# Optimization experiments

Measured on AMD Instinct MI355X. Metric: run time of the kernel, lower is better.

The kernel has to match this reference:

```python
import jax, jax.numpy as jnp
import numpy as np

CHANNELS = [4096, 4096, 4096, 4096]
SPARSITY = 0.9  # fraction of weight entries zeroed (sten.random_mask_sparsify frac)
BATCH = 4096


def _sparse_weight(key, out_f, in_f, frac):
    kw, km = jax.random.split(key)
    w = jax.random.normal(kw, (out_f, in_f), dtype=jnp.float32)
    keep = jax.random.uniform(km, (out_f, in_f)) >= frac  # keep ~(1-frac) entries
    return jnp.where(keep, w, 0.0)


def setup_inputs() -> dict:
    key = jax.random.key(0)
    ks = jax.random.split(key, 7)
    x = jax.random.normal(ks[0], (BATCH, CHANNELS[0]), dtype=jnp.float32)
    W1 = _sparse_weight(ks[1], CHANNELS[1], CHANNELS[0], SPARSITY)
    b1 = jax.random.uniform(ks[2], (CHANNELS[1],), dtype=jnp.float32)
    W2 = _sparse_weight(ks[3], CHANNELS[2], CHANNELS[1], SPARSITY)
    b2 = jax.random.uniform(ks[4], (CHANNELS[2],), dtype=jnp.float32)
    W3 = _sparse_weight(ks[5], CHANNELS[3], CHANNELS[2], SPARSITY)
    b3 = jax.random.uniform(ks[6], (CHANNELS[3],), dtype=jnp.float32)
    return {"x": x, "W1": W1, "b1": b1, "W2": W2, "b2": b2, "W3": W3, "b3": b3}


def reference(x, W1, b1, W2, b2, W3, b3):
    # Sequential: Linear -> ReLU -> Linear -> ReLU -> Linear
    # F.linear(x, W, b) == x @ W.T + b; weights already carry the sparsity mask.
    h = x @ W1.T + b1
    h = jax.nn.relu(h)
    h = h @ W2.T + b2
    h = jax.nn.relu(h)
    return h @ W3.T + b3
```

## Files before the change

### kernel.cpp

```cpp
#include <hip/hip_runtime.h>
#include <cstdint>


#define MATN 4096
#define NT (MATN / 64)

typedef _Float16 half8 __attribute__((ext_vector_type(8)));
typedef float f32x4 __attribute__((ext_vector_type(4)));

__device__ __forceinline__ void glds16(const void* g, void* l) {
    __builtin_amdgcn_global_load_lds(
        (const __attribute__((address_space(1))) char*)(uintptr_t)g,
        (__attribute__((address_space(3))) char*)(uintptr_t)l,
        16, 0, 0);
}

__device__ __forceinline__ void cvt_body(const float* __restrict__ in,
                                         _Float16* __restrict__ out, int n8) {
    for (int g = blockIdx.x * 256 + threadIdx.x; g < n8; g += gridDim.x * 256) {
        size_t i = (size_t)g * 8;
        float4 a = *(const float4*)(in + i);
        float4 b = *(const float4*)(in + i + 4);
        half8 o;
        o[0] = (_Float16)a.x; o[1] = (_Float16)a.y;
        o[2] = (_Float16)a.z; o[3] = (_Float16)a.w;
        o[4] = (_Float16)b.x; o[5] = (_Float16)b.y;
        o[6] = (_Float16)b.z; o[7] = (_Float16)b.w;
        *(half8*)(out + i) = o;
    }
}

__global__ __launch_bounds__(256)
void cvt_f16(const float* __restrict__ in, _Float16* __restrict__ out, int n8) {
    cvt_body(in, out, n8);
}

__global__ __launch_bounds__(256)
void cvt_f16_2(const float* __restrict__ i0, _Float16* __restrict__ o0,
               const float* __restrict__ i1, _Float16* __restrict__ o1, int n8) {
    cvt_body(blockIdx.y ? i1 : i0, blockIdx.y ? o1 : o0, n8);
}

__global__ __launch_bounds__(256)
void cvt_f16_4(const float* __restrict__ i0, _Float16* __restrict__ o0,
               const float* __restrict__ i1, _Float16* __restrict__ o1,
               const float* __restrict__ i2, _Float16* __restrict__ o2,
               const float* __restrict__ i3, _Float16* __restrict__ o3, int n8) {
    const float* in;
    _Float16* out;
    switch (blockIdx.y) {
        case 0: in = i0; out = o0; break;
        case 1: in = i1; out = o1; break;
        case 2: in = i2; out = o2; break;
        default: in = i3; out = o3; break;
    }
    cvt_body(in, out, n8);
}

#define MFMA_(d, x, y) d = __builtin_amdgcn_mfma_f32_16x16x32_f16(x, y, d, 0, 0, 0)

template <bool RELU, typename OutT>
__global__ __launch_bounds__(512, 2)
void gemm_bt(const _Float16* __restrict__ A, const _Float16* __restrict__ B,
             const float* __restrict__ bias, OutT* __restrict__ C) {
    __shared__ _Float16 lds[2][4][128 * 64];

    const int tid  = threadIdx.x;
    const int lane = tid & 63;
    const int w    = tid >> 6;
    const int wm   = w >> 2;
    const int wn   = w & 3;
    const int l16  = lane & 15;
    const int kq   = lane >> 4;

    const int bid   = blockIdx.y * 16 + blockIdx.x;
    const int sbid  = (bid & 7) * 32 + (bid >> 3);
    const int tileM = (sbid >> 4) * 256;
    const int tileN = (sbid & 15) * 256;

    const int rin = tid >> 3;
    const int gch = (tid & 7) ^ (rin & 7);
    char* const ldsb = (char*)lds;
    const int wq = w * 1024;

    const _Float16* const arow = A + (size_t)(tileM + rin) * MATN + gch * 8;
    const _Float16* const brow = B + (size_t)(tileN + rin) * MATN + gch * 8;

#define STAGE(Tt, s, rowp, roff)                                               \
    do {                                                                       \
        if ((Tt) < NT) {                                                       \
            const _Float16* g_ = (rowp) + (size_t)(roff) * MATN + (Tt) * 64;   \
            char* l_ = ldsb + ((((Tt) & 1) * 4 + (s)) * 16384) + wq;           \
            glds16(g_, l_);                                                    \
            glds16(g_ + (size_t)64 * MATN, l_ + 8192);                         \
        }                                                                      \
    } while (0)

    const int rbA = (wm * 16 + l16) * 128;
    const int rbB = (wn * 16 + l16) * 128;
    const int ok0 = (kq ^ (l16 & 7)) * 16;
    const int ok1 = ok0 ^ 64;

    half8 aP[4], aQ[4], bP[4], bQ[4];
    f32x4 acc[8][4] = {};

    STAGE(0, 0, arow, 0);
    STAGE(0, 1, brow, 0);
    STAGE(0, 2, brow, 128);
    STAGE(0, 3, arow, 128);
    STAGE(1, 2, brow, 128);
    asm volatile("s_waitcnt vmcnt(2)" ::: "memory");
    __builtin_amdgcn_s_barrier();

#pragma unroll 2
    for (int T = 0; T < NT; ++T) {
        const char* base  = ldsb + (T & 1) * 65536;
        const char* bufA0 = base;
        const char* bufB0 = base + 16384;
        const char* bufB1 = base + 32768;
        const char* bufA1 = base + 49152;

#pragma unroll
        for (int mi = 0; mi < 4; ++mi)
            aP[mi] = *(const half8*)(bufA0 + mi * 4096 + rbA + ok0);
        bP[0] = *(const half8*)(bufB0 + rbB + ok0);
        bP[1] = *(const half8*)(bufB0 + 8192 + rbB + ok0);
        bP[2] = *(const half8*)(bufB1 + rbB + ok0);
        bP[3] = *(const half8*)(bufB1 + 8192 + rbB + ok0);
#pragma unroll
        for (int mi = 0; mi < 4; ++mi)
            aQ[mi] = *(const half8*)(bufA1 + mi * 4096 + rbA + ok0);
        STAGE(T + 1, 0, arow, 0);
        __builtin_amdgcn_s_barrier();
        asm volatile("s_waitcnt lgkmcnt(4)" ::: "memory");
        __builtin_amdgcn_sched_barrier(0);
        __builtin_amdgcn_s_setprio(1);
#pragma unroll
        for (int mi = 0; mi < 4; ++mi)
#pragma unroll
            for (int ni = 0; ni < 4; ++ni)
                MFMA_(acc[mi][ni], aP[mi], bP[ni]);
        __builtin_amdgcn_s_setprio(0);
        __builtin_amdgcn_s_barrier();

#pragma unroll
        for (int mi = 0; mi < 4; ++mi)
            aP[mi] = *(const half8*)(bufA1 + mi * 4096 + rbA + ok1);
        bQ[0] = *(const half8*)(bufB0 + rbB + ok1);
        bQ[1] = *(const half8*)(bufB0 + 8192 + rbB + ok1);
        bQ[2] = *(const half8*)(bufB1 + rbB + ok1);
        bQ[3] = *(const half8*)(bufB1 + 8192 + rbB + ok1);
        STAGE(T + 1, 3, arow, 128);
        __builtin_amdgcn_s_barrier();
        asm volatile("s_waitcnt lgkmcnt(8)" ::: "memory");
        __builtin_amdgcn_sched_barrier(0);
        __builtin_amdgcn_s_setprio(1);
#pragma unroll
        for (int mi = 0; mi < 4; ++mi)
#pragma unroll
            for (int ni = 0; ni < 4; ++ni)
                MFMA_(acc[4 + mi][ni], aQ[mi], bP[ni]);
        __builtin_amdgcn_s_setprio(0);
        __builtin_amdgcn_s_barrier();

#pragma unroll
        for (int mi = 0; mi < 4; ++mi)
            aQ[mi] = *(const half8*)(bufA0 + mi * 4096 + rbA + ok1);
        STAGE(T + 1, 1, brow, 0);
        __builtin_amdgcn_s_barrier();
        asm volatile("s_waitcnt lgkmcnt(4)" ::: "memory");
        __builtin_amdgcn_sched_barrier(0);
        __builtin_amdgcn_s_setprio(1);
#pragma unroll
        for (int mi = 0; mi < 4; ++mi)
#pragma unroll
            for (int ni = 0; ni < 4; ++ni)
                MFMA_(acc[4 + mi][ni], aP[mi], bQ[ni]);
        __builtin_amdgcn_s_setprio(0);
        __builtin_amdgcn_s_barrier();

        STAGE(T + 2, 2, brow, 128);
        __builtin_amdgcn_s_barrier();
        asm volatile("s_waitcnt lgkmcnt(0)" ::: "memory");
        __builtin_amdgcn_sched_barrier(0);
        __builtin_amdgcn_s_setprio(1);
#pragma unroll
        for (int mi = 0; mi < 4; ++mi)
#pragma unroll
            for (int ni = 0; ni < 4; ++ni)
                MFMA_(acc[mi][ni], aQ[mi], bQ[ni]);
        __builtin_amdgcn_s_setprio(0);
        if (T < NT - 2)
            asm volatile("s_waitcnt vmcnt(2)" ::: "memory");
        else
            asm volatile("s_waitcnt vmcnt(0)" ::: "memory");
        __builtin_amdgcn_s_barrier();
    }
#undef STAGE

#pragma unroll
    for (int ni = 0; ni < 4; ++ni) {
        const int gn = tileN + ni * 64 + wn * 16 + l16;
        const float bv = bias[gn];
#pragma unroll
        for (int mi = 0; mi < 8; ++mi) {
            const int gm = tileM + mi * 32 + wm * 16 + kq * 4;
#pragma unroll
            for (int r = 0; r < 4; ++r) {
                float v = acc[mi][ni][r] + bv;
                if (RELU) v = v > 0.f ? v : 0.f;
                C[(size_t)(gm + r) * MATN + gn] = (OutT)v;
            }
        }
    }
}

extern "C" void kernel_launch(void* const* d_in, const int* in_sizes, int n_in,
                              void* d_out, int out_size, void* d_ws, size_t ws_size,
                              hipStream_t stream) {
    const float* x  = (const float*)d_in[0];
    const float* W1 = (const float*)d_in[1];
    const float* b1 = (const float*)d_in[2];
    const float* W2 = (const float*)d_in[3];
    const float* b2 = (const float*)d_in[4];
    const float* W3 = (const float*)d_in[5];
    const float* b3 = (const float*)d_in[6];
    float* out = (float*)d_out;

    const size_t MAT = (size_t)MATN * MATN;
    const size_t HB  = MAT * 2;
    const int n8 = (int)(MAT / 8);
    dim3 ggrid(MATN / 256, MATN / 256);

    if (ws_size >= HB * 5) {
        _Float16* xb = (_Float16*)d_ws;
        _Float16* w1 = (_Float16*)((char*)d_ws + HB);
        _Float16* w2 = (_Float16*)((char*)d_ws + HB * 2);
        _Float16* w3 = (_Float16*)((char*)d_ws + HB * 3);
        _Float16* h1 = (_Float16*)((char*)d_ws + HB * 4);
        _Float16* h2 = xb;

        cvt_f16_4<<<dim3(2048, 4), 256, 0, stream>>>(x, xb, W1, w1, W2, w2,
                                                     W3, w3, n8);
        gemm_bt<true, _Float16><<<ggrid, 512, 0, stream>>>(xb, w1, b1, h1);
        gemm_bt<true, _Float16><<<ggrid, 512, 0, stream>>>(h1, w2, b2, h2);
        gemm_bt<false, float><<<ggrid, 512, 0, stream>>>(h2, w3, b3, out);
    } else {
        _Float16* xb = (_Float16*)d_ws;
        _Float16* wb = (_Float16*)((char*)d_ws + HB);
        _Float16* h1 = (_Float16*)((char*)d_ws + HB * 2);
        _Float16* h2 = xb;

        cvt_f16_2<<<dim3(2048, 2), 256, 0, stream>>>(x, xb, W1, wb, n8);
        gemm_bt<true, _Float16><<<ggrid, 512, 0, stream>>>(xb, wb, b1, h1);
        cvt_f16<<<2048, 256, 0, stream>>>(W2, wb, n8);
        gemm_bt<true, _Float16><<<ggrid, 512, 0, stream>>>(h1, wb, b2, h2);
        cvt_f16<<<2048, 256, 0, stream>>>(W3, wb, n8);
        gemm_bt<false, float><<<ggrid, 512, 0, stream>>>(h2, wb, b3, out);
    }
}
```

Baseline: 589.0 us.

## Stage tiles in MFMA-fragment order so LDS reads are lane-linear

Each thread now loads from global memory in an order that places data in LDS exactly in the per-lane MFMA fragment layout, replacing the XOR-swizzled row layout. LDS reads become contiguous lane*16 accesses with simple offsets, which avoids bank conflicts and cuts address arithmetic. The warp-to-output mapping changes (each warp owns a contiguous 128x64 block), and the first compute phase now waits for all LDS reads (lgkmcnt(0)). Global loads become less contiguous per row, which may reduce coalescing.

New measurement: 661.1 us. +12.2%, slower.

```diff
diff --git a/kernel.cpp b/kernel.cpp
--- a/kernel.cpp
+++ b/kernel.cpp
@@ -78,59 +78,88 @@
     const int tileM = (sbid >> 4) * 256;
     const int tileN = (sbid & 15) * 256;
 
-    const int rin = tid >> 3;
-    const int gch = (tid & 7) ^ (rin & 7);
     char* const ldsb = (char*)lds;
-    const int wq = w * 1024;
-
-    const _Float16* const arow = A + (size_t)(tileM + rin) * MATN + gch * 8;
-    const _Float16* const brow = B + (size_t)(tileN + rin) * MATN + gch * 8;
-
-#define STAGE(Tt, s, rowp, roff)                                               \
+
+    const int rowStage = ((tid >> 7) & 3) * 16 + l16;
+    const int colStage = (w & 1) * 32 + kq * 8;
+    const _Float16* const aS = A + (size_t)(tileM + rowStage) * MATN + colStage;
+    const _Float16* const bS = B + (size_t)(tileN + rowStage) * MATN + colStage;
+
+#define STAGE_(Tt, reg, half, src)                                             \
     do {                                                                       \
         if ((Tt) < NT) {                                                       \
-            const _Float16* g_ = (rowp) + (size_t)(roff) * MATN + (Tt) * 64;   \
-            char* l_ = ldsb + ((((Tt) & 1) * 4 + (s)) * 16384) + wq;           \
+            const _Float16* g_ =                                               \
+                (src) + (size_t)((half) * 128) * MATN + (Tt) * 64;             \
+            char* l_ = ldsb + (((Tt) & 1) * 4 + (reg)) * 16384 + w * 1024;     \
             glds16(g_, l_);                                                    \
             glds16(g_ + (size_t)64 * MATN, l_ + 8192);                         \
         }                                                                      \
     } while (0)
-
-    const int rbA = (wm * 16 + l16) * 128;
-    const int rbB = (wn * 16 + l16) * 128;
-    const int ok0 = (kq ^ (l16 & 7)) * 16;
-    const int ok1 = ok0 ^ 64;
+#define STAGE_A(Tt, mh) STAGE_(Tt, (mh) * 3, mh, aS)
+#define STAGE_B(Tt, nh) STAGE_(Tt, 1 + (nh), nh, bS)
 
     half8 aP[4], aQ[4], bP[4], bQ[4];
     f32x4 acc[8][4] = {};
 
-    STAGE(0, 0, arow, 0);
-    STAGE(0, 1, brow, 0);
-    STAGE(0, 2, brow, 128);
-    STAGE(0, 3, arow, 128);
-    STAGE(1, 2, brow, 128);
+    STAGE_A(0, 0);
+    STAGE_B(0, 0);
+    STAGE_B(0, 1);
+    STAGE_A(0, 1);
+    STAGE_B(1, 1);
     asm volatile("s_waitcnt vmcnt(2)" ::: "memory");
     __builtin_amdgcn_s_barrier();
 
 #pragma unroll 2
     for (int T = 0; T < NT; ++T) {
-        const char* base  = ldsb + (T & 1) * 65536;
-        const char* bufA0 = base;
-        const char* bufB0 = base + 16384;
-        const char* bufB1 = base + 32768;
-        const char* bufA1 = base + 49152;
-
-#pragma unroll
-        for (int mi = 0; mi < 4; ++mi)
-            aP[mi] = *(const half8*)(bufA0 + mi * 4096 + rbA + ok0);
-        bP[0] = *(const half8*)(bufB0 + rbB + ok0);
-        bP[1] = *(const half8*)(bufB0 + 8192 + rbB + ok0);
-        bP[2] = *(const half8*)(bufB1 + rbB + ok0);
-        bP[3] = *(const half8*)(bufB1 + 8192 + rbB + ok0);
-#pragma unroll
-        for (int mi = 0; mi < 4; ++mi)
-            aQ[mi] = *(const half8*)(bufA1 + mi * 4096 + rbA + ok0);
-        STAGE(T + 1, 0, arow, 0);
+        const char* Ard = ldsb + (T & 1) * 65536 + wm * 3 * 16384 + lane * 16;
+        const char* Brd = ldsb + (T & 1) * 65536 + (1 + (wn >> 1)) * 16384 +
+                          (wn & 1) * 8192 + lane * 16;
+
+#pragma unroll
+        for (int mi = 0; mi < 4; ++mi)
+            aP[mi] = *(const half8*)(Ard + mi * 2048);
+#pragma unroll
+        for (int ni = 0; ni < 4; ++ni)
+            bP[ni] = *(const half8*)(Brd + ni * 2048);
+#pragma unroll
+        for (int mi = 0; mi < 4; ++mi)
+            aQ[mi] = *(const half8*)(Ard + 8192 + mi * 2048);
+        STAGE_A(T + 1, 0);
+        __builtin_amdgcn_s_barrier();
+        asm volatile("s_waitcnt lgkmcnt(0)" ::: "memory");
+        __builtin_amdgcn_sched_barrier(0);
+        __builtin_amdgcn_s_setprio(1);
+#pragma unroll
+        for (int mi = 0; mi < 4; ++mi)
+#pragma unroll
+            for (int ni = 0; ni < 4; ++ni)
+                MFMA_(acc[mi][ni], aP[mi], bP[ni]);
+        __builtin_amdgcn_s_setprio(0);
+        __builtin_amdgcn_s_barrier();
+
+#pragma unroll
+        for (int mi = 0; mi < 4; ++mi)
+            aP[mi] = *(const half8*)(Ard + 8192 + mi * 2048 + 1024);
+#pragma unroll
+        for (int ni = 0; ni < 4; ++ni)
+            bQ[ni] = *(const half8*)(Brd + ni * 2048 + 1024);
+        STAGE_A(T + 1, 1);
+        __builtin_amdgcn_s_barrier();
+        asm volatile("s_waitcnt lgkmcnt(8)" ::: "memory");
+        __builtin_amdgcn_sched_barrier(0);
+        __builtin_amdgcn_s_setprio(1);
+#pragma unroll
+        for (int mi = 0; mi < 4; ++mi)
+#pragma unroll
+            for (int ni = 0; ni < 4; ++ni)
+                MFMA_(acc[4 + mi][ni], aQ[mi], bP[ni]);
+        __builtin_amdgcn_s_setprio(0);
+        __builtin_amdgcn_s_barrier();
+
+#pragma unroll
+        for (int mi = 0; mi < 4; ++mi)
+            aQ[mi] = *(const half8*)(Ard + mi * 2048 + 1024);
+        STAGE_B(T + 1, 0);
         __builtin_amdgcn_s_barrier();
         asm volatile("s_waitcnt lgkmcnt(4)" ::: "memory");
         __builtin_amdgcn_sched_barrier(0);
@@ -139,47 +168,11 @@
         for (int mi = 0; mi < 4; ++mi)
 #pragma unroll
             for (int ni = 0; ni < 4; ++ni)
-                MFMA_(acc[mi][ni], aP[mi], bP[ni]);
-        __builtin_amdgcn_s_setprio(0);
-        __builtin_amdgcn_s_barrier();
-
-#pragma unroll
-        for (int mi = 0; mi < 4; ++mi)
-            aP[mi] = *(const half8*)(bufA1 + mi * 4096 + rbA + ok1);
-        bQ[0] = *(const half8*)(bufB0 + rbB + ok1);
-        bQ[1] = *(const half8*)(bufB0 + 8192 + rbB + ok1);
-        bQ[2] = *(const half8*)(bufB1 + rbB + ok1);
-        bQ[3] = *(const half8*)(bufB1 + 8192 + rbB + ok1);
-        STAGE(T + 1, 3, arow, 128);
-        __builtin_amdgcn_s_barrier();
-        asm volatile("s_waitcnt lgkmcnt(8)" ::: "memory");
-        __builtin_amdgcn_sched_barrier(0);
-        __builtin_amdgcn_s_setprio(1);
-#pragma unroll
-        for (int mi = 0; mi < 4; ++mi)
-#pragma unroll
-            for (int ni = 0; ni < 4; ++ni)
-                MFMA_(acc[4 + mi][ni], aQ[mi], bP[ni]);
-        __builtin_amdgcn_s_setprio(0);
-        __builtin_amdgcn_s_barrier();
-
-#pragma unroll
-        for (int mi = 0; mi < 4; ++mi)
-            aQ[mi] = *(const half8*)(bufA0 + mi * 4096 + rbA + ok1);
-        STAGE(T + 1, 1, brow, 0);
-        __builtin_amdgcn_s_barrier();
-        asm volatile("s_waitcnt lgkmcnt(4)" ::: "memory");
-        __builtin_amdgcn_sched_barrier(0);
-        __builtin_amdgcn_s_setprio(1);
-#pragma unroll
-        for (int mi = 0; mi < 4; ++mi)
-#pragma unroll
-            for (int ni = 0; ni < 4; ++ni)
                 MFMA_(acc[4 + mi][ni], aP[mi], bQ[ni]);
         __builtin_amdgcn_s_setprio(0);
         __builtin_amdgcn_s_barrier();
 
-        STAGE(T + 2, 2, brow, 128);
+        STAGE_B(T + 2, 1);
         __builtin_amdgcn_s_barrier();
         asm volatile("s_waitcnt lgkmcnt(0)" ::: "memory");
         __builtin_amdgcn_sched_barrier(0);
@@ -196,15 +189,17 @@
             asm volatile("s_waitcnt vmcnt(0)" ::: "memory");
         __builtin_amdgcn_s_barrier();
     }
-#undef STAGE
+#undef STAGE_A
+#undef STAGE_B
+#undef STAGE_
 
 #pragma unroll
     for (int ni = 0; ni < 4; ++ni) {
-        const int gn = tileN + ni * 64 + wn * 16 + l16;
+        const int gn = tileN + wn * 64 + ni * 16 + l16;
         const float bv = bias[gn];
 #pragma unroll
         for (int mi = 0; mi < 8; ++mi) {
-            const int gm = tileM + mi * 32 + wm * 16 + kq * 4;
+            const int gm = tileM + wm * 128 + mi * 16 + kq * 4;
 #pragma unroll
             for (int r = 0; r < 4; ++r) {
                 float v = acc[mi][ni][r] + bv;
```
